# Kernel optimization log

Measured on AMD Instinct MI355X. Metric: run time of the kernel, lower is better.

## Reference

```python
import jax, jax.numpy as jnp
import numpy as np

N = 20000       # nodes
E = 500000      # edges
D = 256         # dim_in == dim_out (residual requires equality)
T = 4           # num_layers
NTYPES = 3      # cfg.edge_types = [0, 1, 2]
NU = 1          # cfg nu; nu_v2 = False -> delay = max(k - NU, 0) = k - 1


def setup_inputs() -> dict:
    key = jax.random.key(0)
    ks = jax.random.split(key, 8)
    x = jax.random.normal(ks[0], (N, D), dtype=jnp.float32)
    edge_index = jax.random.randint(ks[1], (2, E), 0, N, dtype=jnp.int32)
    hop = jax.random.randint(ks[2], (E,), 1, T + 1, dtype=jnp.int32)   # k in 1..T
    etype = jax.random.randint(ks[3], (E,), 0, NTYPES, dtype=jnp.int32)
    edge_attr = jnp.stack([hop, etype], axis=1)  # [E, 2]
    scale = 0.05
    W_edge = scale * jax.random.normal(ks[4], (T, NTYPES, D, D), dtype=jnp.float32)
    b_edge = scale * jax.random.normal(ks[5], (T, NTYPES, D), dtype=jnp.float32)
    # hop layers W(k, t) for k in 2..t+1; index (t, k-2); max k = T -> T-1 slots
    W_hop = scale * jax.random.normal(ks[6], (T, T - 1, D, D), dtype=jnp.float32)
    b_hop = scale * jax.random.normal(ks[7], (T, T - 1, D), dtype=jnp.float32)
    return {"x": x, "edge_index": edge_index, "edge_attr": edge_attr,
            "W_edge": W_edge, "b_edge": b_edge, "W_hop": W_hop, "b_hop": b_hop}


def _gnn_layer(h_src, src, dst, mask, n_nodes):
    # GNNLayer: linear transform at source nodes then sum-aggregate over the
    # masked edge subset (equivalent to restricting edge_index to that subset).
    msg = jnp.where(mask[:, None], h_src[src], jnp.float32(0.0))  # [E, D]
    return jax.ops.segment_sum(msg, dst, num_segments=n_nodes)    # [N, D]


def reference(x, edge_index, edge_attr, W_edge, b_edge, W_hop, b_hop):
    n_nodes = x.shape[0]
    src, dst = edge_index[0], edge_index[1]
    hop, etype = edge_attr[:, 0], edge_attr[:, 1]
    xs = []
    for t in range(T):
        xs.append(x)
        acc = jnp.zeros_like(x)
        # 1-hop relational layers, one per edge type e
        for e in range(NTYPES):
            h = xs[t] @ W_edge[t, e] + b_edge[t, e]          # transform at node level
            acc = acc + _gnn_layer(h, src, dst, etype == e, n_nodes)
        # delayed multi-hop layers, k = 2..t+1, reading x[t - delay]
        for k in range(2, t + 2):
            delay = max(k - NU, 0)  # nu_v2 = False
            h = xs[t - delay] @ W_hop[t, k - 2] + b_hop[t, k - 2]
            acc = acc + _gnn_layer(h, src, dst, hop == k, n_nodes)
        x = xs[t] + jax.nn.relu(acc)  # residual; cfg.gnn.l2norm = False
    return x
```

## Files before the change

kernel.cpp:

```cpp
#include <hip/hip_runtime.h>


#define NN 20000
#define NE 500000
#define DD 256
#define TT 4
#define NT 3
#define BK 32
#define NB 118

typedef _Float16 f16;
typedef _Float16 f16x8 __attribute__((ext_vector_type(8)));
typedef _Float16 f16x4v __attribute__((ext_vector_type(4)));
typedef float f32x4 __attribute__((ext_vector_type(4)));

__device__ inline void f4add(float4& a, const float4 b) {
  a.x += b.x; a.y += b.y; a.z += b.z; a.w += b.w;
}

__device__ __forceinline__ void gload_lds16(const void* g, void* l) {
  __builtin_amdgcn_global_load_lds(
      (const __attribute__((address_space(1))) unsigned int*)g,
      (__attribute__((address_space(3))) unsigned int*)l, 16, 0, 0);
}


__global__ void k_hist(const int* __restrict__ ei, const int* __restrict__ ea,
                       int* __restrict__ cnt) {
  int e = blockIdx.x * 256 + threadIdx.x;
  if (e >= NE) return;
  int dst = ei[NE + e];
  int hop = ea[2 * e];
  int et  = ea[2 * e + 1];
  atomicAdd(&cnt[et * NN + dst], 1);
  if (hop >= 2) atomicAdd(&cnt[(3 + hop - 2) * NN + dst], 1);
}


__global__ __launch_bounds__(1024) void k_scan_blk(
    const int* __restrict__ cnt, int* __restrict__ crow, int* __restrict__ bsum) {
  __shared__ int wsum[16];
  int tid = threadIdx.x, lane = tid & 63, wv = tid >> 6;
  int i = blockIdx.x * 1024 + tid;
  int v = (i < 6 * NN) ? cnt[i] : 0;
  int s = v;
#pragma unroll
  for (int off = 1; off < 64; off <<= 1) {
    int t = __shfl_up(s, off, 64);
    if (lane >= off) s += t;
  }
  if (lane == 63) wsum[wv] = s;
  __syncthreads();
  if (wv == 0) {
    int ws = (lane < 16) ? wsum[lane] : 0;
#pragma unroll
    for (int off = 1; off < 16; off <<= 1) {
      int t = __shfl_up(ws, off, 64);
      if (lane >= off) ws += t;
    }
    if (lane < 16) wsum[lane] = ws;
  }
  __syncthreads();
  int excl = ((wv == 0) ? 0 : wsum[wv - 1]) + s - v;
  if (i < 6 * NN) crow[i] = excl;
  if (tid == 1023) bsum[blockIdx.x] = wsum[15];
}

__global__ __launch_bounds__(128) void k_scan_top(
    int* __restrict__ bsum, int* __restrict__ crow) {
  __shared__ int wsum2[2];
  int tid = threadIdx.x, lane = tid & 63, wv = tid >> 6;
  int v = (tid < NB) ? bsum[tid] : 0;
  int s = v;
#pragma unroll
  for (int off = 1; off < 64; off <<= 1) {
    int t = __shfl_up(s, off, 64);
    if (lane >= off) s += t;
  }
  if (lane == 63) wsum2[wv] = s;
  __syncthreads();
  int add = (wv == 1) ? wsum2[0] : 0;
  int excl = add + s - v;
  if (tid < NB) bsum[tid] = excl;
  if (tid == NB - 1) crow[6 * NN] = excl + v;
}

__global__ __launch_bounds__(1024) void k_scan_fix(
    int* __restrict__ crow, int* __restrict__ ccur, const int* __restrict__ bsum) {
  int i = blockIdx.x * 1024 + threadIdx.x;
  if (i >= 6 * NN) return;
  int val = crow[i] + bsum[blockIdx.x];
  crow[i] = val;
  ccur[i] = val;
}

__global__ void k_scatter(const int* __restrict__ ei, const int* __restrict__ ea,
                          int* __restrict__ ccur, int* __restrict__ crec) {
  int e = blockIdx.x * 256 + threadIdx.x;
  if (e >= NE) return;
  int src = ei[e];
  int dst = ei[NE + e];
  int hop = ea[2 * e];
  int et  = ea[2 * e + 1];
  int pos = atomicAdd(&ccur[et * NN + dst], 1);
  crec[pos] = src;
  if (hop >= 2) {
    int pos2 = atomicAdd(&ccur[(3 + hop - 2) * NN + dst], 1);
    crec[pos2] = src;
  }
}


__global__ __launch_bounds__(256) void k_wsplit(
    const float* __restrict__ W_edge, const float* __restrict__ W_hop,
    f16* __restrict__ Wout) {
  __shared__ float tile[64][65];
  int w = blockIdx.z;
  int tk = blockIdx.x * 64;
  int tn = blockIdx.y * 64;
  const float* src = (w < 12) ? (W_edge + (size_t)w * 65536)
                              : (W_hop + (size_t)(w - 12) * 65536);
  f16* dst = Wout + (size_t)w * 65536;
  int c = threadIdx.x & 63;
  int r0 = threadIdx.x >> 6;
#pragma unroll
  for (int i = 0; i < 16; i++) {
    int r = i * 4 + r0;
    tile[r][c] = src[(size_t)(tk + r) * 256 + tn + c] * 16.0f;
  }
  __syncthreads();
#pragma unroll
  for (int i = 0; i < 16; i++) {
    int r = i * 4 + r0;
    dst[(size_t)(tn + r) * 256 + tk + c] = (f16)tile[c][r];
  }
}


__global__ void k_xcast(const float* __restrict__ x, f16* __restrict__ xh) {
  size_t i = (size_t)(blockIdx.x * 256 + threadIdx.x) * 4;
  float4 v = *(const float4*)(x + i);
  f16x4v h = { (f16)v.x, (f16)v.y, (f16)v.z, (f16)v.w };
  *(f16x4v*)(xh + i) = h;
}


__device__ inline void store_h(f16* __restrict__ p, float4 v) {
  const float s = 0.015625f;
  f16x4v h = { (f16)(v.x * s), (f16)(v.y * s), (f16)(v.z * s), (f16)(v.w * s) };
  *(f16x4v*)p = h;
}

__device__ __forceinline__ float4 cvt4(f16x4v h) {
  return make_float4((float)h.x, (float)h.y, (float)h.z, (float)h.w);
}

struct AggArgs {
  f16* out[6];
};

__global__ __launch_bounds__(256) void k_aggregate(
    const f16* __restrict__ xh,
    const int* __restrict__ crow,
    const int* __restrict__ crec,
    AggArgs args)
{
  int ch = blockIdx.y;
  f16* outp = args.out[ch];
  if (!outp) return;
  int wave = threadIdx.x >> 6;
  int lane = threadIdx.x & 63;
  int v = blockIdx.x * 4 + wave;
  int base = ch * NN + v;
  int beg = crow[base], end = crow[base + 1];
  const f16* xb = xh + (lane << 2);
  float4 acc = make_float4(0, 0, 0, 0);
  int e = beg;
  for (; e + 4 <= end; e += 4) {
    int s0 = crec[e], s1 = crec[e + 1], s2 = crec[e + 2], s3 = crec[e + 3];
    f16x4v h0 = *(const f16x4v*)(xb + (size_t)s0 * DD);
    f16x4v h1 = *(const f16x4v*)(xb + (size_t)s1 * DD);
    f16x4v h2 = *(const f16x4v*)(xb + (size_t)s2 * DD);
    f16x4v h3 = *(const f16x4v*)(xb + (size_t)s3 * DD);
    float4 t0 = cvt4(h0), t1 = cvt4(h1), t2 = cvt4(h2), t3 = cvt4(h3);
    f4add(t0, t1);
    f4add(t2, t3);
    f4add(t0, t2);
    f4add(acc, t0);
  }
  for (; e < end; ++e) {
    int s0 = crec[e];
    f16x4v h0 = *(const f16x4v*)(xb + (size_t)s0 * DD);
    f4add(acc, cvt4(h0));
  }
  store_h(outp + (size_t)v * DD + (lane << 2), acc);
}


struct GemmArgs {
  const f16* A[6];
  const f16* W[6];
  const float* bias[6];
  const int*   cnt[6];
  int nch;
  int write_f32;
  const f16* xh_in;
  f16*       xh_out;
  float*     f32_out;
};

__global__ __launch_bounds__(256) void k_gemm(GemmArgs args) {
  __shared__ __align__(16) f16 sA[2][32 * BK];
  __shared__ __align__(16) f16 sB[2][128 * BK];
  const int tid = threadIdx.x;
  const int lane = tid & 63;
  const int wave = tid >> 6;
  const int wm = (wave >> 1) * 16;
  const int wn = (wave & 1) * 64;
  const int m0 = blockIdx.x * 32;
  const int n0 = blockIdx.y * 128;
  const int nch = args.nch;
  const int T = nch * 8;

  f32x4 acc[4];
#pragma unroll
  for (int j = 0; j < 4; j++) acc[j] = (f32x4){0.f, 0.f, 0.f, 0.f};

  const bool doA = (tid < 128);
  const int ar = (tid & 127) >> 2, aq = tid & 3;
  const int agS = ar * 512 + ((aq ^ ((ar >> 1) & 3)) << 4);
  char* const ldsA[2] = { (char*)sA[0] + (tid & 127) * 16,
                          (char*)sA[1] + (tid & 127) * 16 };
  int bgS[2];
  char* ldsBp[2][2];
#pragma unroll
  for (int i = 0; i < 2; i++) {
    int s = i * 256 + tid;
    int r = s >> 2, q = s & 3;
    bgS[i] = r * 512 + ((q ^ ((r >> 1) & 3)) << 4);
    ldsBp[0][i] = (char*)sB[0] + s * 16;
    ldsBp[1][i] = (char*)sB[1] + s * 16;
  }

  const int fr = lane & 15;
  const int gq = lane >> 4;
  int offA, offB[4];
  {
    int rr = wm + fr;
    offA = rr * BK + ((gq ^ ((rr >> 1) & 3)) << 3);
  }
#pragma unroll
  for (int ni = 0; ni < 4; ni++) {
    int rr = wn + ni * 16 + fr;
    offB[ni] = rr * BK + ((gq ^ ((rr >> 1) & 3)) << 3);
  }

  {
    const char* pa = (const char*)args.A[0] + (size_t)m0 * 512;
    const char* pb = (const char*)args.W[0] + (size_t)n0 * 512;
    if (doA) gload_lds16(pa + agS, ldsA[0]);
    gload_lds16(pb + bgS[0], ldsBp[0][0]);
    gload_lds16(pb + bgS[1], ldsBp[0][1]);
  }
  __syncthreads();

  for (int j = 0; j < T; ++j) {
    const int p = j & 1;
    {
      int jn = (j + 1 < T) ? j + 1 : j;
      int c = jn >> 3, kb = (jn & 7) * 64;
      const char* pa = (const char*)args.A[c] + (size_t)m0 * 512 + kb;
      const char* pb = (const char*)args.W[c] + (size_t)n0 * 512 + kb;
      if (doA) gload_lds16(pa + agS, ldsA[p ^ 1]);
      gload_lds16(pb + bgS[0], ldsBp[p ^ 1][0]);
      gload_lds16(pb + bgS[1], ldsBp[p ^ 1][1]);
    }
    {
      f16x8 fA, fB[4];
      fA = *(const f16x8*)&sA[p][offA];
#pragma unroll
      for (int ni = 0; ni < 4; ni++) fB[ni] = *(const f16x8*)&sB[p][offB[ni]];
#pragma unroll
      for (int ni = 0; ni < 4; ni++)
        acc[ni] = __builtin_amdgcn_mfma_f32_16x16x32_f16(fA, fB[ni], acc[ni], 0, 0, 0);
    }
    __syncthreads();
  }

  float bcol[4][6];
#pragma unroll
  for (int ni = 0; ni < 4; ni++) {
    int gcol = n0 + wn + ni * 16 + fr;
#pragma unroll
    for (int c = 0; c < 6; c++)
      bcol[ni][c] = (c < nch) ? args.bias[c][gcol] : 0.f;
  }
  const int rowq = gq * 4;
#pragma unroll
  for (int rI = 0; rI < 4; rI++) {
    int grow = m0 + wm + rowq + rI;
    float cv[6];
#pragma unroll
    for (int c = 0; c < 6; c++)
      cv[c] = (c < nch) ? (float)args.cnt[c][grow] : 0.f;
    size_t rowoff = (size_t)grow * DD;
#pragma unroll
    for (int ni = 0; ni < 4; ni++) {
      int gcol = n0 + wn + ni * 16 + fr;
      float v = acc[ni][rI] * 4.0f;
#pragma unroll
      for (int c = 0; c < 6; c++) v += cv[c] * bcol[ni][c];
      float outv = (float)args.xh_in[rowoff + gcol] + fmaxf(v, 0.f);
      args.xh_out[rowoff + gcol] = (f16)outv;
      if (args.write_f32) args.f32_out[rowoff + gcol] = outv;
    }
  }
}


extern "C" void kernel_launch(void* const* d_in, const int* in_sizes, int n_in,
                              void* d_out, int out_size, void* d_ws, size_t ws_size,
                              hipStream_t stream) {
  const float* x      = (const float*)d_in[0];
  const int* edge_index = (const int*)d_in[1];
  const int* edge_attr  = (const int*)d_in[2];
  const float* W_edge = (const float*)d_in[3];
  const float* b_edge = (const float*)d_in[4];
  const float* W_hop  = (const float*)d_in[5];
  const float* b_hop  = (const float*)d_in[6];
  float* out = (float*)d_out;

  char* ws = (char*)d_ws;
  int* cnt  = (int*)ws;
  int* crow = cnt + 6 * NN;
  int* ccur = crow + 6 * NN + 1;
  int* bsum = ccur + 6 * NN;
  int* crec = bsum + NB;
  size_t int_count = (size_t)6 * NN + (6 * NN + 1) + 6 * NN + NB + 2 * (size_t)NE;
  const size_t ND = (size_t)NN * DD;
  f16* Wsplit = (f16*)(ws + ((int_count * 4 + 255) & ~(size_t)255));
  f16* xh = Wsplit + (size_t)24 * 65536;
  f16* aggBase = xh + ND;
  f16* agg[9];
  for (int i = 0; i < 9; i++) agg[i] = aggBase + (size_t)i * ND;
  f16** Cb = agg + 3;

  hipMemsetAsync(cnt, 0, 6 * NN * sizeof(int), stream);

  k_hist<<<(NE + 255) / 256, 256, 0, stream>>>(edge_index, edge_attr, cnt);
  k_scan_blk<<<NB, 1024, 0, stream>>>(cnt, crow, bsum);
  k_scan_top<<<1, 128, 0, stream>>>(bsum, crow);
  k_scan_fix<<<NB, 1024, 0, stream>>>(crow, ccur, bsum);
  k_scatter<<<(NE + 255) / 256, 256, 0, stream>>>(edge_index, edge_attr, ccur, crec);
  k_wsplit<<<dim3(4, 4, 24), 256, 0, stream>>>(W_edge, W_hop, Wsplit);
  k_xcast<<<ND / 1024, 256, 0, stream>>>(x, xh);

  for (int t = 0; t < TT; ++t) {
    AggArgs aa{};
    aa.out[0] = agg[0];
    aa.out[1] = agg[1];
    aa.out[2] = agg[2];
    aa.out[3] = (t <= 2) ? Cb[t]     : nullptr;
    aa.out[4] = (t <= 1) ? Cb[3 + t] : nullptr;
    aa.out[5] = (t == 0) ? Cb[5]     : nullptr;
    k_aggregate<<<dim3(NN / 4, 6), 256, 0, stream>>>(xh, crow, crec, aa);

    GemmArgs ga{};
    for (int e = 0; e < NT; ++e) {
      ga.A[e]    = agg[e];
      ga.W[e]    = Wsplit + (size_t)(t * NT + e) * 65536;
      ga.bias[e] = b_edge + (size_t)(t * NT + e) * DD;
      ga.cnt[e]  = cnt + (size_t)e * NN;
    }
    int nc = NT;
    for (int k = 2; k <= t + 1; ++k) {
      int s = t + 1 - k;
      ga.A[nc]    = (k == 2) ? Cb[s] : (k == 3) ? Cb[3 + s] : Cb[5];
      ga.W[nc]    = Wsplit + (size_t)(12 + t * 3 + (k - 2)) * 65536;
      ga.bias[nc] = b_hop + (size_t)(t * (TT - 1) + (k - 2)) * DD;
      ga.cnt[nc]  = cnt + (size_t)(3 + (k - 2)) * NN;
      nc++;
    }
    for (int c = nc; c < 6; ++c) {
      ga.A[c] = ga.A[0]; ga.W[c] = ga.W[0]; ga.bias[c] = ga.bias[0]; ga.cnt[c] = ga.cnt[0];
    }
    ga.nch = nc;
    ga.write_f32 = (t == TT - 1) ? 1 : 0;
    ga.xh_in  = xh;
    ga.xh_out = xh;
    ga.f32_out = out;
    k_gemm<<<dim3(625, 2), 256, 0, stream>>>(ga);
  }
}
```

Measured before the change: 558.0 us.

## Enlarge GEMM tile to 64x128 with BK=64 and pad aggregate buffers

The fused GEMM kernel moves from 32-row to 64-row tiles, and the K step per stage grows from 32 to 64 (two MFMA k-slices). Each wave now computes 2x4 MFMA blocks, which roughly halves the number of blocks and barriers and gives more reuse per loaded B tile. The aggregate buffers are padded to 20032 rows so the last tile can read past row 20000 without going out of bounds, and stores are guarded by row. In exchange the kernel uses more LDS and registers per block, which may lower occupancy, and the padded rows are read without being initialised.

```diff
diff --git a/kernel.cpp b/kernel.cpp
--- a/kernel.cpp
+++ b/kernel.cpp
@@ -2,11 +2,11 @@
 
 
 #define NN 20000
+#define NROWP 20032
 #define NE 500000
 #define DD 256
 #define TT 4
 #define NT 3
-#define BK 32
 #define NB 118
 
 typedef _Float16 f16;
@@ -210,80 +210,100 @@
 };
 
 __global__ __launch_bounds__(256) void k_gemm(GemmArgs args) {
-  __shared__ __align__(16) f16 sA[2][32 * BK];
-  __shared__ __align__(16) f16 sB[2][128 * BK];
+  __shared__ __align__(16) f16 sA[2][4096];
+  __shared__ __align__(16) f16 sB[2][8192];
   const int tid = threadIdx.x;
   const int lane = tid & 63;
   const int wave = tid >> 6;
-  const int wm = (wave >> 1) * 16;
+  const int wm = (wave >> 1) * 32;
   const int wn = (wave & 1) * 64;
-  const int m0 = blockIdx.x * 32;
+  const int m0 = blockIdx.x * 64;
   const int n0 = blockIdx.y * 128;
   const int nch = args.nch;
-  const int T = nch * 8;
-
-  f32x4 acc[4];
-#pragma unroll
-  for (int j = 0; j < 4; j++) acc[j] = (f32x4){0.f, 0.f, 0.f, 0.f};
-
-  const bool doA = (tid < 128);
-  const int ar = (tid & 127) >> 2, aq = tid & 3;
-  const int agS = ar * 512 + ((aq ^ ((ar >> 1) & 3)) << 4);
-  char* const ldsA[2] = { (char*)sA[0] + (tid & 127) * 16,
-                          (char*)sA[1] + (tid & 127) * 16 };
-  int bgS[2];
-  char* ldsBp[2][2];
+  const int Titer = nch * 4;
+
+  f32x4 acc[2][4];
+#pragma unroll
+  for (int mi = 0; mi < 2; mi++)
+#pragma unroll
+    for (int ni = 0; ni < 4; ni++) acc[mi][ni] = (f32x4){0.f, 0.f, 0.f, 0.f};
+
+  int srcA[2], ldsAoff[2];
 #pragma unroll
   for (int i = 0; i < 2; i++) {
-    int s = i * 256 + tid;
-    int r = s >> 2, q = s & 3;
-    bgS[i] = r * 512 + ((q ^ ((r >> 1) & 3)) << 4);
-    ldsBp[0][i] = (char*)sB[0] + s * 16;
-    ldsBp[1][i] = (char*)sB[1] + s * 16;
+    int g = wave + i * 4;
+    int s = g * 64 + lane;
+    int ks = s >> 8, r = (s >> 2) & 63, pc = s & 3;
+    int lc = pc ^ ((r >> 1) & 3);
+    srcA[i] = r * 512 + ks * 64 + lc * 16;
+    ldsAoff[i] = g * 1024;
+  }
+  int srcB[4], ldsBoff[4];
+#pragma unroll
+  for (int i = 0; i < 4; i++) {
+    int g = wave + i * 4;
+    int s = g * 64 + lane;
+    int ks = s >> 9, r = (s >> 2) & 127, pc = s & 3;
+    int lc = pc ^ ((r >> 1) & 3);
+    srcB[i] = r * 512 + ks * 64 + lc * 16;
+    ldsBoff[i] = g * 1024;
   }
 
   const int fr = lane & 15;
   const int gq = lane >> 4;
-  int offA, offB[4];
-  {
-    int rr = wm + fr;
-    offA = rr * BK + ((gq ^ ((rr >> 1) & 3)) << 3);
+  int offA[2][2], offB[4][2];
+#pragma unroll
+  for (int mi = 0; mi < 2; mi++) {
+    int rr = wm + mi * 16 + fr;
+    int swz = (gq ^ ((rr >> 1) & 3)) << 4;
+#pragma unroll
+    for (int ks = 0; ks < 2; ks++) offA[mi][ks] = ks * 4096 + rr * 64 + swz;
   }
 #pragma unroll
   for (int ni = 0; ni < 4; ni++) {
     int rr = wn + ni * 16 + fr;
-    offB[ni] = rr * BK + ((gq ^ ((rr >> 1) & 3)) << 3);
-  }
-
-  {
-    const char* pa = (const char*)args.A[0] + (size_t)m0 * 512;
-    const char* pb = (const char*)args.W[0] + (size_t)n0 * 512;
-    if (doA) gload_lds16(pa + agS, ldsA[0]);
-    gload_lds16(pb + bgS[0], ldsBp[0][0]);
-    gload_lds16(pb + bgS[1], ldsBp[0][1]);
-  }
+    int swz = (gq ^ ((rr >> 1) & 3)) << 4;
+#pragma unroll
+    for (int ks = 0; ks < 2; ks++) offB[ni][ks] = ks * 8192 + rr * 64 + swz;
+  }
+
+  auto stage = [&](int buf, int j) {
+    int c = j >> 2, kb = (j & 3) * 128;
+    const char* pa = (const char*)args.A[c] + (size_t)m0 * 512 + kb;
+    const char* pb = (const char*)args.W[c] + (size_t)n0 * 512 + kb;
+#pragma unroll
+    for (int i = 0; i < 2; i++)
+      gload_lds16(pa + srcA[i], (char*)sA[buf] + ldsAoff[i]);
+#pragma unroll
+    for (int i = 0; i < 4; i++)
+      gload_lds16(pb + srcB[i], (char*)sB[buf] + ldsBoff[i]);
+  };
+
+  stage(0, 0);
   __syncthreads();
 
-  for (int j = 0; j < T; ++j) {
+  for (int j = 0; j < Titer; ++j) {
     const int p = j & 1;
-    {
-      int jn = (j + 1 < T) ? j + 1 : j;
-      int c = jn >> 3, kb = (jn & 7) * 64;
-      const char* pa = (const char*)args.A[c] + (size_t)m0 * 512 + kb;
-      const char* pb = (const char*)args.W[c] + (size_t)n0 * 512 + kb;
-      if (doA) gload_lds16(pa + agS, ldsA[p ^ 1]);
-      gload_lds16(pb + bgS[0], ldsBp[p ^ 1][0]);
-      gload_lds16(pb + bgS[1], ldsBp[p ^ 1][1]);
-    }
-    {
-      f16x8 fA, fB[4];
-      fA = *(const f16x8*)&sA[p][offA];
-#pragma unroll
-      for (int ni = 0; ni < 4; ni++) fB[ni] = *(const f16x8*)&sB[p][offB[ni]];
+    int jn = (j + 1 < Titer) ? j + 1 : j;
+    stage(p ^ 1, jn);
+    f16x8 fA[2][2], fB[2][4];
+#pragma unroll
+    for (int ks = 0; ks < 2; ks++) {
+#pragma unroll
+      for (int mi = 0; mi < 2; mi++)
+        fA[ks][mi] = *(const f16x8*)((const char*)sA[p] + offA[mi][ks]);
 #pragma unroll
       for (int ni = 0; ni < 4; ni++)
-        acc[ni] = __builtin_amdgcn_mfma_f32_16x16x32_f16(fA, fB[ni], acc[ni], 0, 0, 0);
-    }
+        fB[ks][ni] = *(const f16x8*)((const char*)sB[p] + offB[ni][ks]);
+    }
+#pragma unroll
+    for (int ks = 0; ks < 2; ks++)
+#pragma unroll
+      for (int mi = 0; mi < 2; mi++)
+#pragma unroll
+        for (int ni = 0; ni < 4; ni++)
+          acc[mi][ni] = __builtin_amdgcn_mfma_f32_16x16x32_f16(
+              fA[ks][mi], fB[ks][ni], acc[mi][ni], 0, 0, 0);
     __syncthreads();
   }
 
@@ -297,22 +317,27 @@
   }
   const int rowq = gq * 4;
 #pragma unroll
-  for (int rI = 0; rI < 4; rI++) {
-    int grow = m0 + wm + rowq + rI;
-    float cv[6];
-#pragma unroll
-    for (int c = 0; c < 6; c++)
-      cv[c] = (c < nch) ? (float)args.cnt[c][grow] : 0.f;
-    size_t rowoff = (size_t)grow * DD;
-#pragma unroll
-    for (int ni = 0; ni < 4; ni++) {
-      int gcol = n0 + wn + ni * 16 + fr;
-      float v = acc[ni][rI] * 4.0f;
-#pragma unroll
-      for (int c = 0; c < 6; c++) v += cv[c] * bcol[ni][c];
-      float outv = (float)args.xh_in[rowoff + gcol] + fmaxf(v, 0.f);
-      args.xh_out[rowoff + gcol] = (f16)outv;
-      if (args.write_f32) args.f32_out[rowoff + gcol] = outv;
+  for (int mi = 0; mi < 2; mi++) {
+#pragma unroll
+    for (int rI = 0; rI < 4; rI++) {
+      int grow = m0 + wm + mi * 16 + rowq + rI;
+      if (grow < NN) {
+        float cv[6];
+#pragma unroll
+        for (int c = 0; c < 6; c++)
+          cv[c] = (c < nch) ? (float)args.cnt[c][grow] : 0.f;
+        size_t rowoff = (size_t)grow * DD;
+#pragma unroll
+        for (int ni = 0; ni < 4; ni++) {
+          int gcol = n0 + wn + ni * 16 + fr;
+          float v = acc[mi][ni][rI] * 4.0f;
+#pragma unroll
+          for (int c = 0; c < 6; c++) v += cv[c] * bcol[ni][c];
+          float outv = (float)args.xh_in[rowoff + gcol] + fmaxf(v, 0.f);
+          args.xh_out[rowoff + gcol] = (f16)outv;
+          if (args.write_f32) args.f32_out[rowoff + gcol] = outv;
+        }
+      }
     }
   }
 }
@@ -337,12 +362,13 @@
   int* bsum = ccur + 6 * NN;
   int* crec = bsum + NB;
   size_t int_count = (size_t)6 * NN + (6 * NN + 1) + 6 * NN + NB + 2 * (size_t)NE;
-  const size_t ND = (size_t)NN * DD;
+  const size_t ND  = (size_t)NN * DD;
+  const size_t NDP = (size_t)NROWP * DD;
   f16* Wsplit = (f16*)(ws + ((int_count * 4 + 255) & ~(size_t)255));
   f16* xh = Wsplit + (size_t)24 * 65536;
   f16* aggBase = xh + ND;
   f16* agg[9];
-  for (int i = 0; i < 9; i++) agg[i] = aggBase + (size_t)i * ND;
+  for (int i = 0; i < 9; i++) agg[i] = aggBase + (size_t)i * NDP;
   f16** Cb = agg + 3;
 
   hipMemsetAsync(cnt, 0, 6 * NN * sizeof(int), stream);
@@ -389,6 +415,6 @@
     ga.xh_in  = xh;
     ga.xh_out = xh;
     ga.f32_out = out;
-    k_gemm<<<dim3(625, 2), 256, 0, stream>>>(ga);
-  }
-}
+    k_gemm<<<dim3(313, 2), 256, 0, stream>>>(ga);
+  }
+}
```

Result: faster. 544.3 us (-2.5%).
